# Performance work log

Measured on AMD Instinct MI355X. Metric: run time of the kernel, lower is better.

Reference implementation:

```python
import jax, jax.numpy as jnp
import numpy as np

HID = 768
NUM_HEADS = 12
HEAD_DIM = HID // NUM_HEADS
MASK_VALUE = -1.0e9
EPS = 1.0e-4  # module's self.eps, also used as the diagonal fill constant


def setup_inputs() -> dict:
    key = jax.random.key(0)
    k1, k2, k3 = jax.random.split(key, 3)
    B, M = 16, 512
    ocr_features = jax.random.normal(k1, (B, M, HID), dtype=jnp.float32)
    # prior neighbor-attention from previous layer, probabilities in [0,1)
    prior = jax.random.uniform(k2, (B, 1, M, M), dtype=jnp.float32)
    Wq = jax.random.normal(k3, (HID, HID), dtype=jnp.float32) / np.sqrt(HID)
    bq = jnp.zeros((HID,), dtype=jnp.float32)
    ocr_features_mask = jnp.ones((B, M), dtype=jnp.int32)
    return {"ocr_features": ocr_features, "prior": prior, "Wq": Wq, "bq": bq,
            "ocr_features_mask": ocr_features_mask}


def reference(ocr_features, prior, Wq, bq, ocr_features_mask):
    B, M, _ = ocr_features.shape
    # Module uses q_linear for Q, K (and V, which is unused) -> Q == K.
    q = (ocr_features @ Wq + bq).reshape(B, M, NUM_HEADS, HEAD_DIM)
    q = q.transpose(0, 2, 1, 3)  # (B, H, M, D)
    # note: scaled by head_dim (not sqrt), as in the source
    scores = jnp.einsum('bhid,bhjd->bhij', q, q) / HEAD_DIM  # (B, H, M, M)

    dt = scores.dtype
    prev_word_mask = jnp.eye(M, k=1, dtype=dt)   # superdiagonal
    next_word_mask = jnp.eye(M, k=-1, dtype=dt)  # subdiagonal
    main_diag_mask = jnp.eye(M, dtype=dt)

    # neighbor mask: only prev/next word positions that are valid OCR tokens
    neibor_mask = ((prev_word_mask + next_word_mask)[None, :, :] > 0) & \
                  (ocr_features_mask[:, None, :] > 0)  # (B, M, M)
    scores = jnp.where(neibor_mask[:, None, :, :], scores, MASK_VALUE)
    neibor_attn = jax.nn.softmax(scores, axis=-1)
    # symmetrize: sqrt(a * a^T + eps)
    neibor_attn = jnp.sqrt(neibor_attn * jnp.swapaxes(neibor_attn, -1, -2) + EPS)
    neibor_attn = prior + (1.0 - prior) * neibor_attn

    # log-space cumulative product via triangular matmuls
    tri = jnp.triu(jnp.ones((M, M), dtype=dt))  # (M, M), incl. diagonal
    # keep only superdiagonal log-probs, cumulative-sum to the right via tri
    t = jnp.where(prev_word_mask > 0, jnp.log(neibor_attn + 1e-9), 0.0) @ tri
    g_attn = jnp.exp(jnp.einsum('ij,bhjk->bhik', tri, t))
    # zero out diagonal and lower triangle (tri - diag == 0 there)
    g_attn = jnp.where((tri - main_diag_mask) > 0, g_attn, 0.0)
    g_attn = g_attn + jnp.swapaxes(g_attn, -1, -2) + \
             jnp.where(main_diag_mask > 0, neibor_attn, EPS)
    return (g_attn, neibor_attn)
```

## Files before the change

kernel.cpp:

```cpp
#include <hip/hip_runtime.h>
#include <cstdint>
#include <cstddef>

#define B_   16
#define M_   512
#define HID_ 768
#define NH_  12
#define HD_  64

typedef short s16x8 __attribute__((ext_vector_type(8)));
typedef float f32x4 __attribute__((ext_vector_type(4)));

__device__ __forceinline__ unsigned short f2bf(float f) {
    unsigned int u = __builtin_bit_cast(unsigned int, f);
    u = u + 0x7FFFu + ((u >> 16) & 1u);
    return (unsigned short)(u >> 16);
}

__launch_bounds__(256)
__global__ void gemm_q(const float* __restrict__ X, const float* __restrict__ W,
                       const float* __restrict__ bq, float* __restrict__ Q) {
    __shared__ unsigned short As[128][40];
    __shared__ unsigned short Bs[128][40];

    const int tid  = threadIdx.x;
    const int lane = tid & 63;
    const int wave = tid >> 6;
    const int wr   = (wave >> 1) * 64;
    const int wc   = (wave & 1) * 64;
    const int ln   = lane & 15;
    const int quad = lane >> 4;
    const int q8   = quad * 8;
    const int r0   = blockIdx.y * 128;
    const int n0   = blockIdx.x * 128;

    f32x4 acc[4][4] = {};

    for (int kt = 0; kt < HID_ / 32; ++kt) {
        const int k0 = kt * 32;
        #pragma unroll
        for (int p = 0; p < 4; ++p) {
            int t = tid + p * 256;
            int row = t >> 3;
            int kk  = (t & 7) * 4;
            const float4 v = *(const float4*)(X + (size_t)(r0 + row) * HID_ + k0 + kk);
            As[row][kk + 0] = f2bf(v.x);
            As[row][kk + 1] = f2bf(v.y);
            As[row][kk + 2] = f2bf(v.z);
            As[row][kk + 3] = f2bf(v.w);
        }
        #pragma unroll
        for (int p = 0; p < 4; ++p) {
            int t = tid + p * 256;
            int kr = t >> 5;
            int nn = (t & 31) * 4;
            const float4 v = *(const float4*)(W + (size_t)(k0 + kr) * HID_ + n0 + nn);
            Bs[nn + 0][kr] = f2bf(v.x);
            Bs[nn + 1][kr] = f2bf(v.y);
            Bs[nn + 2][kr] = f2bf(v.z);
            Bs[nn + 3][kr] = f2bf(v.w);
        }
        __syncthreads();

        s16x8 af[4], bf[4];
        #pragma unroll
        for (int r = 0; r < 4; ++r)
            af[r] = *(const s16x8*)&As[wr + r * 16 + ln][q8];
        #pragma unroll
        for (int c = 0; c < 4; ++c)
            bf[c] = *(const s16x8*)&Bs[wc + c * 16 + ln][q8];
        #pragma unroll
        for (int r = 0; r < 4; ++r)
            #pragma unroll
            for (int c = 0; c < 4; ++c)
                acc[r][c] = __builtin_amdgcn_mfma_f32_16x16x32_bf16(af[r], bf[c], acc[r][c], 0, 0, 0);
        __syncthreads();
    }

    #pragma unroll
    for (int c = 0; c < 4; ++c) {
        const int col = n0 + wc + c * 16 + ln;
        const float bias = bq[col];
        #pragma unroll
        for (int r = 0; r < 4; ++r) {
            const int rowb = r0 + wr + r * 16 + quad * 4;
            #pragma unroll
            for (int e = 0; e < 4; ++e)
                Q[(size_t)(rowb + e) * HID_ + col] = acc[r][c][e] + bias;
        }
    }
}

__launch_bounds__(512)
__global__ void rowstats(const float* __restrict__ Q, const float* __restrict__ prior,
                         const int* __restrict__ mask,
                         float* __restrict__ na_super, float* __restrict__ na_sub,
                         float* __restrict__ Ssum) {
    const int bh = blockIdx.x;
    const int b  = bh / NH_;
    const int h  = bh - b * NH_;
    const int i  = threadIdx.x;

    __shared__ float sh_s[M_];
    __shared__ float sh_pp[M_];
    __shared__ float sc[2][M_];

    float s = 0.f;
    if (i < M_ - 1) {
        const float4* qa = (const float4*)(Q + (size_t)(b * M_ + i)     * HID_ + h * HD_);
        const float4* qb = (const float4*)(Q + (size_t)(b * M_ + i + 1) * HID_ + h * HD_);
        #pragma unroll
        for (int t = 0; t < 16; ++t) {
            float4 x = qa[t], y = qb[t];
            s += x.x * y.x + x.y * y.y + x.z * y.z + x.w * y.w;
        }
        s *= (1.f / 64.f);
    }
    sh_s[i] = s;
    __syncthreads();

    const bool vp = (i > 0)      && (mask[b * M_ + i - 1] > 0);
    const bool vn = (i < M_ - 1) && (mask[b * M_ + i + 1] > 0);
    const float sp = vp ? sh_s[i - 1] : -1e30f;
    const float sn = vn ? s : -1e30f;
    const float mx = fmaxf(sp, sn);
    const float ep = vp ? __expf(sp - mx) : 0.f;
    const float en = vn ? __expf(sn - mx) : 0.f;
    float den = ep + en;
    den = (den > 0.f) ? den : 1.f;
    const float pp = ep / den;
    const float pn = en / den;
    sh_pp[i] = pp;
    __syncthreads();

    float Lv = 0.f;
    if (i < M_ - 1) {
        const float  sym = sqrtf(pn * sh_pp[i + 1] + 1e-4f);
        const size_t pb  = (size_t)b * (M_ * M_);
        const float  prs = prior[pb + (size_t)i * M_ + (i + 1)];
        const float  prb = prior[pb + (size_t)(i + 1) * M_ + i];
        const float  nsup = prs + (1.f - prs) * sym;
        na_super[bh * M_ + i] = nsup;
        na_sub[bh * M_ + i]   = prb + (1.f - prb) * sym;
        Lv = logf(nsup + 1e-9f);
    }

    int pbuf = 0;
    sc[0][i] = Lv;
    __syncthreads();
    for (int off = 1; off < M_; off <<= 1) {
        float v = sc[pbuf][i] + ((i >= off) ? sc[pbuf][i - off] : 0.f);
        sc[pbuf ^ 1][i] = v;
        __syncthreads();
        pbuf ^= 1;
    }
    Ssum[bh * M_ + i] = (i > 0) ? sc[pbuf][i - 1] : 0.f;
}

__launch_bounds__(256)
__global__ void fill_out(const float* __restrict__ prior,
                         const float* __restrict__ na_super,
                         const float* __restrict__ na_sub,
                         const float* __restrict__ Ssum,
                         float* __restrict__ out) {
    const int tid = threadIdx.x;
    const int idx = blockIdx.x * 2 + (tid >> 7);
    const int h   = idx % NH_;
    const int tmp = idx / NH_;
    const int i   = tmp & (M_ - 1);
    const int b   = tmp >> 9;
    const int bh  = b * NH_ + h;
    const int j0  = (tid & 127) * 4;

    const float4 pr4 = *(const float4*)(prior + (size_t)b * (M_ * M_) + (size_t)i * M_ + j0);
    const float4 S4  = *(const float4*)(Ssum + bh * M_ + j0);
    const float  Si  = Ssum[bh * M_ + i];
    const float  nsup_i   = (i < M_ - 1) ? na_super[bh * M_ + i]     : 0.f;
    const float  nsub_im1 = (i > 0)      ? na_sub[bh * M_ + i - 1]   : 0.f;

    const float c0 = 0.00999999977f;

    const float pv[4] = {pr4.x, pr4.y, pr4.z, pr4.w};
    const float sv[4] = {S4.x, S4.y, S4.z, S4.w};
    float nav[4], ggv[4];
    #pragma unroll
    for (int e = 0; e < 4; ++e) {
        const int j = j0 + e;
        float na = fmaf(pv[e], 1.f - c0, c0);
        if (j == i - 1) na = nsub_im1;
        if (j == i + 1) na = nsup_i;
        const float d = sv[e] - Si;
        float g = __expf((j > i) ? d : -d) + 1e-4f;
        if (j == i) g = na;
        nav[e] = na;
        ggv[e] = g;
    }

    const size_t off  = ((size_t)(bh * M_ + i)) * M_ + j0;
    const size_t half = (size_t)B_ * NH_ * M_ * M_;
    f32x4 g4 = {ggv[0], ggv[1], ggv[2], ggv[3]};
    f32x4 n4 = {nav[0], nav[1], nav[2], nav[3]};
    __builtin_nontemporal_store(g4, (f32x4*)(out + off));
    __builtin_nontemporal_store(n4, (f32x4*)(out + half + off));
}

extern "C" void kernel_launch(void* const* d_in, const int* in_sizes, int n_in,
                              void* d_out, int out_size, void* d_ws, size_t ws_size,
                              hipStream_t stream) {
    const float* X     = (const float*)d_in[0];
    const float* prior = (const float*)d_in[1];
    const float* Wq    = (const float*)d_in[2];
    const float* bq    = (const float*)d_in[3];
    const int*   msk   = (const int*)  d_in[4];
    float* out = (float*)d_out;

    float* Q        = (float*)d_ws;
    float* na_super = Q + (size_t)B_ * M_ * HID_;
    float* na_sub   = na_super + (size_t)B_ * NH_ * M_;
    float* Ssum     = na_sub   + (size_t)B_ * NH_ * M_;

    dim3 gg(HID_ / 128, (B_ * M_) / 128);
    gemm_q<<<gg, 256, 0, stream>>>(X, Wq, bq, Q);

    rowstats<<<B_ * NH_, M_, 0, stream>>>(Q, prior, msk, na_super, na_sub, Ssum);

    fill_out<<<(B_ * NH_ * M_) / 2, 256, 0, stream>>>(prior, na_super, na_sub, Ssum, out);
}
```

Baseline: 516.6 us.

## Pre-convert GEMM operands to bf16 and load tiles via direct global-to-LDS

Adds separate kernels that convert X to bf16 and transpose/convert Wq to a bf16 N-major layout in workspace. The projection GEMM then streams tiles straight into LDS with global_load_lds instead of converting and scattering per element. This removes in-loop conversion and strided LDS writes, but adds two launches and extra workspace traffic. The unpadded LDS layout may also cause bank conflicts on fragment reads.

Result: faster. 484.7 us (-6.2%).

```diff
diff --git a/kernel.cpp b/kernel.cpp
--- a/kernel.cpp
+++ b/kernel.cpp
@@ -10,6 +10,8 @@
 
 typedef short s16x8 __attribute__((ext_vector_type(8)));
 typedef float f32x4 __attribute__((ext_vector_type(4)));
+typedef unsigned short u16x8 __attribute__((ext_vector_type(8)));
+typedef unsigned short u16x4 __attribute__((ext_vector_type(4)));
 
 __device__ __forceinline__ unsigned short f2bf(float f) {
     unsigned int u = __builtin_bit_cast(unsigned int, f);
@@ -17,11 +19,49 @@
     return (unsigned short)(u >> 16);
 }
 
-__launch_bounds__(256)
-__global__ void gemm_q(const float* __restrict__ X, const float* __restrict__ W,
-                       const float* __restrict__ bq, float* __restrict__ Q) {
-    __shared__ unsigned short As[128][40];
-    __shared__ unsigned short Bs[128][40];
+__device__ __forceinline__ void gld_lds16(const void* g, void* lds) {
+    __builtin_amdgcn_global_load_lds(
+        (const __attribute__((address_space(1))) unsigned int*)g,
+        (__attribute__((address_space(3))) unsigned int*)lds,
+        16, 0, 0);
+}
+
+__launch_bounds__(256)
+__global__ void convert_x(const float* __restrict__ X, unsigned short* __restrict__ Xb) {
+    const size_t i = ((size_t)blockIdx.x * 256 + threadIdx.x) * 8;
+    const float4 a = *(const float4*)(X + i);
+    const float4 b = *(const float4*)(X + i + 4);
+    u16x8 v = { f2bf(a.x), f2bf(a.y), f2bf(a.z), f2bf(a.w),
+                f2bf(b.x), f2bf(b.y), f2bf(b.z), f2bf(b.w) };
+    *(u16x8*)(Xb + i) = v;
+}
+
+__launch_bounds__(256)
+__global__ void transpose_w(const float* __restrict__ W, unsigned short* __restrict__ Wt) {
+    __shared__ float T[32][33];
+    const int t  = threadIdx.x;
+    const int n0 = blockIdx.x * 32;
+    const int k0 = blockIdx.y * 32;
+    #pragma unroll
+    for (int p = 0; p < 4; ++p) {
+        const int r = p * 8 + (t >> 5);
+        const int c = t & 31;
+        T[r][c] = W[(size_t)(k0 + r) * HID_ + n0 + c];
+    }
+    __syncthreads();
+    const int nl = t >> 3;
+    const int k4 = (t & 7) * 4;
+    u16x4 v = { f2bf(T[k4 + 0][nl]), f2bf(T[k4 + 1][nl]),
+                f2bf(T[k4 + 2][nl]), f2bf(T[k4 + 3][nl]) };
+    *(u16x4*)(Wt + (size_t)(n0 + nl) * HID_ + k0 + k4) = v;
+}
+
+__launch_bounds__(256)
+__global__ void gemm_qb(const unsigned short* __restrict__ Xb,
+                        const unsigned short* __restrict__ Wt,
+                        const float* __restrict__ bq, float* __restrict__ Q) {
+    __shared__ unsigned short As[128 * 32];
+    __shared__ unsigned short Bs[128 * 32];
 
     const int tid  = threadIdx.x;
     const int lane = tid & 63;
@@ -30,45 +70,32 @@
     const int wc   = (wave & 1) * 64;
     const int ln   = lane & 15;
     const int quad = lane >> 4;
-    const int q8   = quad * 8;
     const int r0   = blockIdx.y * 128;
     const int n0   = blockIdx.x * 128;
 
+    const int srow  = lane >> 2;
+    const int skoff = (lane & 3) * 8;
+
     f32x4 acc[4][4] = {};
 
     for (int kt = 0; kt < HID_ / 32; ++kt) {
         const int k0 = kt * 32;
         #pragma unroll
-        for (int p = 0; p < 4; ++p) {
-            int t = tid + p * 256;
-            int row = t >> 3;
-            int kk  = (t & 7) * 4;
-            const float4 v = *(const float4*)(X + (size_t)(r0 + row) * HID_ + k0 + kk);
-            As[row][kk + 0] = f2bf(v.x);
-            As[row][kk + 1] = f2bf(v.y);
-            As[row][kk + 2] = f2bf(v.z);
-            As[row][kk + 3] = f2bf(v.w);
-        }
-        #pragma unroll
-        for (int p = 0; p < 4; ++p) {
-            int t = tid + p * 256;
-            int kr = t >> 5;
-            int nn = (t & 31) * 4;
-            const float4 v = *(const float4*)(W + (size_t)(k0 + kr) * HID_ + n0 + nn);
-            Bs[nn + 0][kr] = f2bf(v.x);
-            Bs[nn + 1][kr] = f2bf(v.y);
-            Bs[nn + 2][kr] = f2bf(v.z);
-            Bs[nn + 3][kr] = f2bf(v.w);
+        for (int c = wave * 2; c < wave * 2 + 2; ++c) {
+            const unsigned short* ga = Xb + (size_t)(r0 + c * 16 + srow) * HID_ + k0 + skoff;
+            gld_lds16(ga, (char*)As + c * 1024);
+            const unsigned short* gb = Wt + (size_t)(n0 + c * 16 + srow) * HID_ + k0 + skoff;
+            gld_lds16(gb, (char*)Bs + c * 1024);
         }
         __syncthreads();
 
         s16x8 af[4], bf[4];
         #pragma unroll
         for (int r = 0; r < 4; ++r)
-            af[r] = *(const s16x8*)&As[wr + r * 16 + ln][q8];
+            af[r] = *(const s16x8*)((const char*)As + (wr + r * 16 + ln) * 64 + quad * 16);
         #pragma unroll
         for (int c = 0; c < 4; ++c)
-            bf[c] = *(const s16x8*)&Bs[wc + c * 16 + ln][q8];
+            bf[c] = *(const s16x8*)((const char*)Bs + (wc + c * 16 + ln) * 64 + quad * 16);
         #pragma unroll
         for (int r = 0; r < 4; ++r)
             #pragma unroll
@@ -218,9 +245,14 @@
     float* na_super = Q + (size_t)B_ * M_ * HID_;
     float* na_sub   = na_super + (size_t)B_ * NH_ * M_;
     float* Ssum     = na_sub   + (size_t)B_ * NH_ * M_;
+    unsigned short* Xb = (unsigned short*)(Ssum + (size_t)B_ * NH_ * M_);
+    unsigned short* Wt = Xb + (size_t)B_ * M_ * HID_;
+
+    convert_x<<<(B_ * M_ * HID_) / (256 * 8), 256, 0, stream>>>(X, Xb);
+    transpose_w<<<dim3(HID_ / 32, HID_ / 32), 256, 0, stream>>>(Wq, Wt);
 
     dim3 gg(HID_ / 128, (B_ * M_) / 128);
-    gemm_q<<<gg, 256, 0, stream>>>(X, Wq, bq, Q);
+    gemm_qb<<<gg, 256, 0, stream>>>(Xb, Wt, bq, Q);
 
     rowstats<<<B_ * NH_, M_, 0, stream>>>(Q, prior, msk, na_super, na_sub, Ssum);
 
```
